# Kernel optimization log

Measured on AMD Instinct MI355X. Metric: run time of the kernel, lower is better.

## Reference

```python
import jax, jax.numpy as jnp
import numpy as np

B, N, C = 8, 8192, 512
H, DH = 8, C // 8
SCALE = 0.02


def setup_inputs() -> dict:
    key = jax.random.key(0)
    k0, k1, k2, k3, k4 = jax.random.split(key, 5)
    return {
        "x": jax.random.normal(k0, (B, N, C), dtype=jnp.float32),
        "w1": SCALE * jax.random.normal(k1, (2, H, DH, DH), dtype=jnp.float32),
        "b1": SCALE * jax.random.normal(k2, (2, H, DH), dtype=jnp.float32),
        "w2": SCALE * jax.random.normal(k3, (2, H, DH, DH), dtype=jnp.float32),
        "b2": SCALE * jax.random.normal(k4, (2, H, DH), dtype=jnp.float32),
    }


def reference(x, w1, b1, w2, b2):
    dtype = x.dtype
    x = x.astype(jnp.float32)
    b, n, c = x.shape
    xf = jnp.fft.rfft(x, axis=1, norm="ortho")            # [B, N//2+1, C] complex
    xf = xf.reshape(b, n // 2 + 1, H, DH)                  # [B, F, H, DH]
    xr, xi = jnp.real(xf), jnp.imag(xf)
    # per-head complex linear 1 + GELU (complex mult split into real/imag)
    o1r = jax.nn.gelu(
        jnp.einsum("bfhi,hio->bfho", xr, w1[0])
        - jnp.einsum("bfhi,hio->bfho", xi, w1[1]) + b1[0], approximate=False)
    o1i = jax.nn.gelu(
        jnp.einsum("bfhi,hio->bfho", xi, w1[0])
        + jnp.einsum("bfhi,hio->bfho", xr, w1[1]) + b1[1], approximate=False)
    # per-head complex linear 2
    o2r = (jnp.einsum("bfhi,hio->bfho", o1r, w2[0])
           - jnp.einsum("bfhi,hio->bfho", o1i, w2[1]) + b2[0])
    o2i = (jnp.einsum("bfhi,hio->bfho", o1i, w2[0])
           + jnp.einsum("bfhi,hio->bfho", o1r, w2[1]) + b2[1])
    yf = (o2r + 1j * o2i).reshape(b, n // 2 + 1, c)
    y = jnp.fft.irfft(yf, n=n, axis=1, norm="ortho")
    return y.astype(dtype)
```

## Files before the change

kernel.cpp:

```cpp
#include <hip/hip_runtime.h>
#include <math.h>

#define BB    8
#define NLEN  8192
#define CC    512
#define HH    8
#define DH    64
#define MH    4096
#define FREQ  4097
#define FP    4104
#define NSEQ  (BB*CC)

#define REGION_BYTES ((size_t)NSEQ * FP * 4ull)

static __device__ __align__(256) unsigned char g_scratch[2ull * (size_t)NSEQ * FP * 4ull];
__device__ unsigned short g_wprep[8 * 4 * 64 * 64];

typedef __attribute__((ext_vector_type(8))) short bf16x8;
typedef __attribute__((ext_vector_type(4))) float f32x4;

__device__ __forceinline__ f32x4 MFMA(bf16x8 a, bf16x8 b, f32x4 c){
  return __builtin_amdgcn_mfma_f32_16x16x32_bf16(a, b, c, 0, 0, 0);
}

__device__ __forceinline__ unsigned short f2bf(float f){
  unsigned u = __float_as_uint(f);
  return (unsigned short)((u + 0x7fffu + ((u >> 16) & 1u)) >> 16);
}
__device__ __forceinline__ unsigned pack2(float a, float b){
  return (unsigned)f2bf(a) | ((unsigned)f2bf(b) << 16);
}
__device__ __forceinline__ float bflo(unsigned u){ return __uint_as_float(u << 16); }
__device__ __forceinline__ float bfhi(unsigned u){ return __uint_as_float(u & 0xffff0000u); }

__device__ __forceinline__ float gelu_fast(float v){
  float x  = v * 0.70710678118654752440f;
  float ax = fabsf(x);
  float t  = __builtin_amdgcn_rcpf(fmaf(0.3275911f, ax, 1.0f));
  float p  = fmaf(fmaf(fmaf(fmaf(1.061405429f, t, -1.453152027f), t,
                            1.421413741f), t, -0.284496736f), t, 0.254829592f);
  float e  = __expf(-x * x);
  float erf_ax = fmaf(-p * t, e, 1.0f);
  float erfx = copysignf(erf_ax, x);
  return 0.5f * v * (1.0f + erfx);
}

__device__ __forceinline__ float2 cadd(float2 a, float2 b){ return make_float2(a.x+b.x, a.y+b.y); }
__device__ __forceinline__ float2 csub(float2 a, float2 b){ return make_float2(a.x-b.x, a.y-b.y); }
__device__ __forceinline__ float2 cmul(float2 a, float2 b){
  return make_float2(fmaf(a.x, b.x, -(a.y*b.y)), fmaf(a.x, b.y, a.y*b.x));
}

__global__ __launch_bounds__(256) void transpose_in_k(const float* __restrict__ in,
                                                      unsigned* __restrict__ out){
  __shared__ float tile[64][33];
  int b  = blockIdx.z;
  int c0 = blockIdx.x * 32;
  int n0 = blockIdx.y * 64;
  int t  = threadIdx.x;
  int tx = t & 31, ty = t >> 5;
  const float* src = in + ((size_t)b * NLEN + n0) * CC + c0;
  #pragma unroll
  for (int k = 0; k < 8; ++k)
    tile[ty + 8*k][tx] = src[(size_t)(ty + 8*k) * CC + tx];
  __syncthreads();
  int lt = t & 15;
  int nl = 4 * lt;
  #pragma unroll
  for (int kk = 0; kk < 2; ++kk){
    int cl = (t >> 4) + 16*kk;
    uint2 u;
    u.x = pack2(tile[nl    ][cl], tile[nl + 1][cl]);
    u.y = pack2(tile[nl + 2][cl], tile[nl + 3][cl]);
    *(uint2*)(out + ((size_t)(b * CC + c0 + cl) * NLEN + n0) / 2 + 2*lt) = u;
  }
}

__global__ __launch_bounds__(256) void transpose_out_k(const unsigned* __restrict__ in,
                                                       float* __restrict__ out){
  __shared__ float tile[64][33];
  int b  = blockIdx.z;
  int c0 = blockIdx.x * 32;
  int n0 = blockIdx.y * 64;
  int t  = threadIdx.x;
  int lt = t & 15;
  int nl = 4 * lt;
  #pragma unroll
  for (int kk = 0; kk < 2; ++kk){
    int cl = (t >> 4) + 16*kk;
    uint2 u = *(const uint2*)(in + ((size_t)(b * CC + c0 + cl) * NLEN + n0) / 2 + 2*lt);
    tile[nl    ][cl] = bflo(u.x);
    tile[nl + 1][cl] = bfhi(u.x);
    tile[nl + 2][cl] = bflo(u.y);
    tile[nl + 3][cl] = bfhi(u.y);
  }
  __syncthreads();
  int tx = t & 31, ty = t >> 5;
  float* dst = out + ((size_t)b * NLEN + n0) * CC + c0;
  #pragma unroll
  for (int k = 0; k < 8; ++k)
    dst[(size_t)(ty + 8*k) * CC + tx] = tile[ty + 8*k][tx];
}

#define SL(e) ((e) + ((e) >> 4))
#define PERM16(p) ((((p) & 3) << 2) | ((p) >> 2))

template<int SIGN>
__device__ __forceinline__ void dft4ip(float2& v0, float2& v1, float2& v2, float2& v3){
  float2 s02 = cadd(v0, v2), d02 = csub(v0, v2);
  float2 s13 = cadd(v1, v3), d13 = csub(v1, v3);
  float2 id = make_float2(-(float)SIGN * d13.y, (float)SIGN * d13.x);
  v0 = cadd(s02, s13);
  v1 = cadd(d02, id);
  v2 = csub(s02, s13);
  v3 = csub(d02, id);
}

template<int SIGN>
__device__ __forceinline__ float2 w16c(int m){
  const float c1 = 0.9238795325112867f, s1 = 0.3826834323650898f, r = 0.7071067811865476f;
  float cs = 1.f, sn = 0.f;
  if (m == 1){ cs = c1;  sn = s1; }
  else if (m == 2){ cs = r;   sn = r; }
  else if (m == 3){ cs = s1;  sn = c1; }
  else if (m == 4){ cs = 0.f; sn = 1.f; }
  else if (m == 6){ cs = -r;  sn = r; }
  else if (m == 9){ cs = -c1; sn = -s1; }
  return make_float2(cs, (float)SIGN * sn);
}

template<int SIGN>
__device__ __forceinline__ void dft16ip(float2 v[16]){
  #pragma unroll
  for (int q0 = 0; q0 < 4; ++q0) dft4ip<SIGN>(v[q0], v[q0+4], v[q0+8], v[q0+12]);
  #pragma unroll
  for (int p0 = 0; p0 < 4; ++p0)
    #pragma unroll
    for (int q0 = 0; q0 < 4; ++q0){
      const int m = p0 * q0;
      if (m) v[q0 + 4*p0] = cmul(v[q0 + 4*p0], w16c<SIGN>(m));
    }
  #pragma unroll
  for (int p0 = 0; p0 < 4; ++p0) dft4ip<SIGN>(v[4*p0], v[4*p0+1], v[4*p0+2], v[4*p0+3]);
}

template<int SIGN>
__device__ __forceinline__ void twiddle16(float2 v[16], int jm, float invRNs){
  float ang = (float)SIGN * 6.2831853071795864769f * (float)jm * invRNs;
  float sn, cs; __sincosf(ang, &sn, &cs);
  float2 w1 = make_float2(cs, sn), w = w1;
  #pragma unroll
  for (int q = 1; q < 16; ++q){ v[q] = cmul(v[q], w); w = cmul(w, w1); }
}

template<int SIGN, int NS>
__device__ __forceinline__ void fft_mid_pass(float2* lds2, float2 v[16], int t){
  #pragma unroll
  for (int q = 0; q < 16; ++q) v[q] = lds2[SL(t + 256*q)];
  int jm = t & (NS - 1);
  twiddle16<SIGN>(v, jm, 1.0f / (16.0f * (float)NS));
  dft16ip<SIGN>(v);
  __syncthreads();
  int base = ((t - jm) << 4) + jm;
  #pragma unroll
  for (int p = 0; p < 16; ++p) lds2[SL(base + p*NS)] = v[PERM16(p)];
  __syncthreads();
}

#define ORTHO_S 0.011048543456039806f

__global__ __launch_bounds__(256) void fft_fwd_k(const unsigned* __restrict__ xt,
                                                 unsigned* __restrict__ spec){
  __shared__ float2 lds2[4352];
  int t = threadIdx.x;
  size_t row = blockIdx.x;
  const unsigned* src = xt + row * (NLEN/2);
  float2 v[16];
  #pragma unroll
  for (int q = 0; q < 16; ++q){
    unsigned u = src[t + 256*q];
    v[q] = make_float2(bflo(u), bfhi(u));
  }
  dft16ip<-1>(v);
  #pragma unroll
  for (int p = 0; p < 16; ++p) lds2[SL(16*t + p)] = v[PERM16(p)];
  __syncthreads();
  fft_mid_pass<-1, 16 >(lds2, v, t);
  fft_mid_pass<-1, 256>(lds2, v, t);
  unsigned* dst = spec + row * (size_t)FP;
  #pragma unroll
  for (int q = 0; q < 16; ++q){
    int k = t + 256*q;
    float2 zk = lds2[SL(k)];
    float2 zc = lds2[SL((MH - k) & (MH - 1))];
    float ex = 0.5f*(zk.x + zc.x);
    float ey = 0.5f*(zk.y - zc.y);
    float ux = zk.x - zc.x;
    float uy = zk.y + zc.y;
    float ox =  0.5f*uy;
    float oy = -0.5f*ux;
    float ang = -6.2831853071795864769f * (float)k / (float)NLEN;
    float sn, cs; __sincosf(ang, &sn, &cs);
    float xr = ex + cs*ox - sn*oy;
    float xi = ey + cs*oy + sn*ox;
    dst[k] = pack2(ORTHO_S*xr, ORTHO_S*xi);
  }
  if (t == 0){
    float2 z0 = lds2[SL(0)];
    dst[MH] = pack2(ORTHO_S*(z0.x - z0.y), 0.0f);
  }
}

__global__ __launch_bounds__(256) void fft_inv_k(const unsigned* __restrict__ spec,
                                                 unsigned* __restrict__ yt){
  __shared__ float2 lds2[4352];
  int t = threadIdx.x;
  size_t row = blockIdx.x;
  const unsigned* src = spec + row * (size_t)FP;
  float2 v[16];
  #pragma unroll
  for (int q = 0; q < 16; ++q){
    int k = t + 256*q;
    unsigned uk = src[k];
    unsigned uc = src[MH - k];
    float2 xk = make_float2(bflo(uk), bfhi(uk));
    float2 xc = make_float2(bflo(uc), bfhi(uc));
    if (k == 0){ xk.y = 0.0f; xc.y = 0.0f; }
    float ex = xk.x + xc.x;
    float ey = xk.y - xc.y;
    float dx = xk.x - xc.x;
    float dy = xk.y + xc.y;
    float ang = 6.2831853071795864769f * (float)k / (float)NLEN;
    float sn, cs; __sincosf(ang, &sn, &cs);
    float ox = cs*dx - sn*dy;
    float oy = cs*dy + sn*dx;
    v[q] = make_float2(ex - oy, ey + ox);
  }
  dft16ip<1>(v);
  #pragma unroll
  for (int p = 0; p < 16; ++p) lds2[SL(16*t + p)] = v[PERM16(p)];
  __syncthreads();
  fft_mid_pass<1, 16 >(lds2, v, t);
  fft_mid_pass<1, 256>(lds2, v, t);
  unsigned* dst = yt + row * (NLEN/2);
  #pragma unroll
  for (int q = 0; q < 16; ++q){
    int m = t + 256*q;
    float2 w = lds2[SL(m)];
    dst[m] = pack2(ORTHO_S*w.x, ORTHO_S*w.y);
  }
}

__global__ __launch_bounds__(256) void wprep_k(const float* __restrict__ w1,
                                               const float* __restrict__ w2){
  int t = threadIdx.x;
  int h = blockIdx.x;
  #pragma unroll 4
  for (int u = 0; u < 64; ++u){
    int idx = t + 256*u;
    int p = idx >> 12;
    int o = (idx >> 6) & 63;
    int jj = idx & 63;
    int swo = (o ^ (o >> 3)) & 7;
    int s = (((jj >> 3) ^ swo) << 3) | (jj & 7);
    int i;
    if (p < 2){
      i = s;
    } else {
      int ks = s >> 5, g = (s >> 3) & 3, j = s & 7;
      i = (2*ks + (j >> 2))*16 + 4*g + (j & 3);
    }
    const float* src = (p < 2) ? w1 : w2;
    float v = src[(size_t)(p & 1) * 32768 + (size_t)h * 4096 + i * 64 + o];
    g_wprep[(size_t)h * 16384 + idx] = f2bf(v);
  }
}

__global__ __launch_bounds__(256) void afno_mid_mfma_k(const unsigned* __restrict__ spec_in,
                                                       unsigned* __restrict__ spec_out,
                                                       const float* __restrict__ b1,
                                                       const float* __restrict__ b2){
  __shared__ unsigned short lds[24576];
  const int t  = threadIdx.x;
  const int bx = blockIdx.x, h = blockIdx.y, b = blockIdx.z;
  const int F0 = bx * 64;
  const size_t rowbase = ((size_t)b * HH + h) * DH;
  const int l = t & 63, wv = t >> 6;
  const int lf = l & 15, lg = l >> 4;

  {
    const uint4* gw  = (const uint4*)(g_wprep + (size_t)h * 16384);
    uint4*       sw4 = (uint4*)(lds + 8192);
    #pragma unroll
    for (int u = 0; u < 8; ++u) sw4[t + 256*u] = gw[t + 256*u];
  }
  {
    unsigned u0[8], u1[8];
    #pragma unroll
    for (int it = 0; it < 8; ++it){
      int ci = wv + 4*it;
      int fc = ci & 3, pc = ci >> 2;
      int f  = fc*16 + lf;
      int i0 = pc*8 + lg*2;
      int fglob = F0 + f;
      u0[it] = 0; u1[it] = 0;
      if (fglob < FREQ){
        u0[it] = spec_in[(rowbase + i0    ) * (size_t)FP + fglob];
        u1[it] = spec_in[(rowbase + i0 + 1) * (size_t)FP + fglob];
      }
    }
    #pragma unroll
    for (int it = 0; it < 8; ++it){
      int ci = wv + 4*it;
      int fc = ci & 3, pc = ci >> 2;
      int f  = fc*16 + lf;
      int i0 = pc*8 + lg*2;
      unsigned wr = __builtin_amdgcn_perm(u1[it], u0[it], 0x05040100u);
      unsigned wi = __builtin_amdgcn_perm(u1[it], u0[it], 0x07060302u);
      int swf = (f ^ (f >> 3)) & 7;
      int j0  = ((((i0 >> 3) ^ swf) << 3) | (i0 & 7));
      *(unsigned*)(lds        + f*64 + j0) = wr;
      *(unsigned*)(lds + 4096 + f*64 + j0) = wi;
    }
  }
  __syncthreads();

  const int wf0 = wv * 16;
  const unsigned short* XR  = lds;
  const unsigned short* XI  = lds + 4096;
  const unsigned short* W1R = lds + 8192;
  const unsigned short* W1I = lds + 12288;
  const unsigned short* W2R = lds + 16384;
  const unsigned short* W2I = lds + 20480;

  const f32x4 zz = {0.f, 0.f, 0.f, 0.f};
  f32x4 a1R[4], a1I[4];
  #pragma unroll
  for (int mt = 0; mt < 4; ++mt){ a1R[mt] = zz; a1I[mt] = zz; }

  #pragma unroll
  for (int ks = 0; ks < 2; ++ks){
    int b0 = ks*4 + lg;
    int f  = wf0 + lf;
    int swf = (f ^ (f >> 3)) & 7;
    int offx = f*64 + ((b0 ^ swf) << 3);
    bf16x8 bxr = *(const bf16x8*)(XR + offx);
    bf16x8 bxi = *(const bf16x8*)(XI + offx);
    #pragma unroll
    for (int mt = 0; mt < 4; ++mt){
      int o = mt*16 + lf;
      int swo = (o ^ (o >> 3)) & 7;
      int off = o*64 + ((b0 ^ swo) << 3);
      bf16x8 awr  = *(const bf16x8*)(W1R + off);
      bf16x8 awi  = *(const bf16x8*)(W1I + off);
      bf16x8 awin = awi ^ (short)0x8000;
      a1R[mt] = MFMA(awr,  bxr, a1R[mt]);
      a1R[mt] = MFMA(awin, bxi, a1R[mt]);
      a1I[mt] = MFMA(awi,  bxr, a1I[mt]);
      a1I[mt] = MFMA(awr,  bxi, a1I[mt]);
    }
  }

  bf16x8 aFr[2], aFi[2], aFin[2];
  #pragma unroll
  for (int ks = 0; ks < 2; ++ks){
    unsigned wr_[4], wi_[4];
    #pragma unroll
    for (int half = 0; half < 2; ++half){
      int mt = 2*ks + half;
      float4 br = *(const float4*)(b1 +       (size_t)h*64 + mt*16 + lg*4);
      float4 bi = *(const float4*)(b1 + 512 + (size_t)h*64 + mt*16 + lg*4);
      float vr0 = gelu_fast(a1R[mt][0] + br.x), vr1 = gelu_fast(a1R[mt][1] + br.y);
      float vr2 = gelu_fast(a1R[mt][2] + br.z), vr3 = gelu_fast(a1R[mt][3] + br.w);
      float vi0 = gelu_fast(a1I[mt][0] + bi.x), vi1 = gelu_fast(a1I[mt][1] + bi.y);
      float vi2 = gelu_fast(a1I[mt][2] + bi.z), vi3 = gelu_fast(a1I[mt][3] + bi.w);
      wr_[half*2    ] = pack2(vr0, vr1);
      wr_[half*2 + 1] = pack2(vr2, vr3);
      wi_[half*2    ] = pack2(vi0, vi1);
      wi_[half*2 + 1] = pack2(vi2, vi3);
    }
    unsigned* pr = (unsigned*)&aFr[ks];
    unsigned* pi = (unsigned*)&aFi[ks];
    #pragma unroll
    for (int w = 0; w < 4; ++w){ pr[w] = wr_[w]; pi[w] = wi_[w]; }
    aFin[ks] = aFi[ks] ^ (short)0x8000;
  }

  f32x4 a2R[4], a2I[4];
  #pragma unroll
  for (int nt = 0; nt < 4; ++nt){ a2R[nt] = zz; a2I[nt] = zz; }

  #pragma unroll
  for (int ks = 0; ks < 2; ++ks){
    int b0 = ks*4 + lg;
    #pragma unroll
    for (int nt = 0; nt < 4; ++nt){
      int o2 = nt*16 + lf;
      int swo = (o2 ^ (o2 >> 3)) & 7;
      int off = o2*64 + ((b0 ^ swo) << 3);
      bf16x8 bwr = *(const bf16x8*)(W2R + off);
      bf16x8 bwi = *(const bf16x8*)(W2I + off);
      a2R[nt] = MFMA(aFr[ks],  bwr, a2R[nt]);
      a2R[nt] = MFMA(aFin[ks], bwi, a2R[nt]);
      a2I[nt] = MFMA(aFi[ks],  bwr, a2I[nt]);
      a2I[nt] = MFMA(aFr[ks],  bwi, a2I[nt]);
    }
  }

  int f0 = F0 + wf0 + lg*4;
  if (f0 <= MH){
    #pragma unroll
    for (int nt = 0; nt < 4; ++nt){
      int o2 = nt*16 + lf;
      float b2r = b2[(size_t)h*64 + o2];
      float b2i = b2[512 + (size_t)h*64 + o2];
      uint4 st;
      st.x = pack2(a2R[nt][0] + b2r, a2I[nt][0] + b2i);
      st.y = pack2(a2R[nt][1] + b2r, a2I[nt][1] + b2i);
      st.z = pack2(a2R[nt][2] + b2r, a2I[nt][2] + b2i);
      st.w = pack2(a2R[nt][3] + b2r, a2I[nt][3] + b2i);
      *(uint4*)(spec_out + (rowbase + o2) * (size_t)FP + f0) = st;
    }
  }
}

extern "C" void kernel_launch(void* const* d_in, const int* in_sizes, int n_in,
                              void* d_out, int out_size, void* d_ws, size_t ws_size,
                              hipStream_t stream) {
  const float* x  = (const float*)d_in[0];
  const float* w1 = (const float*)d_in[1];
  const float* b1 = (const float*)d_in[2];
  const float* w2 = (const float*)d_in[3];
  const float* b2 = (const float*)d_in[4];
  float* out = (float*)d_out;

  unsigned char* base = (unsigned char*)d_ws;
  if (ws_size < 2 * REGION_BYTES){
    void* p = nullptr;
    hipGetSymbolAddress(&p, HIP_SYMBOL(g_scratch));
    base = (unsigned char*)p;
  }
  unsigned* specA = (unsigned*)base;
  unsigned char* regB = base + REGION_BYTES;
  unsigned* xt    = (unsigned*)regB;
  unsigned* specB = (unsigned*)regB;
  unsigned* ytp   = (unsigned*)base;

  wprep_k<<<8, 256, 0, stream>>>(w1, w2);
  transpose_in_k<<<dim3(CC/32, NLEN/64, BB), 256, 0, stream>>>(x, xt);
  fft_fwd_k<<<NSEQ, 256, 0, stream>>>(xt, specA);
  afno_mid_mfma_k<<<dim3(65, HH, BB), 256, 0, stream>>>(specA, specB, b1, b2);
  fft_inv_k<<<NSEQ, 256, 0, stream>>>(specB, ytp);
  transpose_out_k<<<dim3(CC/32, NLEN/64, BB), 256, 0, stream>>>(ytp, out);
}
```

Baseline: 213.7 us.

## Cut sincos calls in FFT kernels and read MLP weights directly from global

The FFT twiddle chain changes from a serial complex-multiply recurrence to a binary-split product tree, which shortens the dependency chain. The per-element sincos in the real-FFT pre/post-processing is replaced by one sincos per thread, rotated by a constant table of 32nd roots of unity. The AFNO MLP kernel stops staging the per-head weights in LDS and loads them straight from global/L2, shrinking LDS from 48KB to 16KB. All three kernels also get launch_bounds min-blocks of 4. Together these aim to cut transcendental work and raise occupancy, at the cost of more global traffic for the weights and possible register pressure or spills.

```diff
diff --git a/kernel.cpp b/kernel.cpp
--- a/kernel.cpp
+++ b/kernel.cpp
@@ -32,6 +32,15 @@
 }
 __device__ __forceinline__ float bflo(unsigned u){ return __uint_as_float(u << 16); }
 __device__ __forceinline__ float bfhi(unsigned u){ return __uint_as_float(u & 0xffff0000u); }
+
+__device__ const float C32C[16] = {
+  1.f, 0.98078528f, 0.92387953f, 0.83146961f, 0.70710678f, 0.55557023f,
+  0.38268343f, 0.19509032f, 0.f, -0.19509032f, -0.38268343f, -0.55557023f,
+  -0.70710678f, -0.83146961f, -0.92387953f, -0.98078528f};
+__device__ const float C32S[16] = {
+  0.f, 0.19509032f, 0.38268343f, 0.55557023f, 0.70710678f, 0.83146961f,
+  0.92387953f, 0.98078528f, 1.f, 0.98078528f, 0.92387953f, 0.83146961f,
+  0.70710678f, 0.55557023f, 0.38268343f, 0.19509032f};
 
 __device__ __forceinline__ float gelu_fast(float v){
   float x  = v * 0.70710678118654752440f;
@@ -148,9 +157,12 @@
 __device__ __forceinline__ void twiddle16(float2 v[16], int jm, float invRNs){
   float ang = (float)SIGN * 6.2831853071795864769f * (float)jm * invRNs;
   float sn, cs; __sincosf(ang, &sn, &cs);
-  float2 w1 = make_float2(cs, sn), w = w1;
-  #pragma unroll
-  for (int q = 1; q < 16; ++q){ v[q] = cmul(v[q], w); w = cmul(w, w1); }
+  float2 tw[16];
+  tw[1] = make_float2(cs, sn);
+  #pragma unroll
+  for (int q = 2; q < 16; ++q) tw[q] = cmul(tw[q >> 1], tw[q - (q >> 1)]);
+  #pragma unroll
+  for (int q = 1; q < 16; ++q) v[q] = cmul(v[q], tw[q]);
 }
 
 template<int SIGN, int NS>
@@ -169,8 +181,8 @@
 
 #define ORTHO_S 0.011048543456039806f
 
-__global__ __launch_bounds__(256) void fft_fwd_k(const unsigned* __restrict__ xt,
-                                                 unsigned* __restrict__ spec){
+__global__ __launch_bounds__(256, 4) void fft_fwd_k(const unsigned* __restrict__ xt,
+                                                    unsigned* __restrict__ spec){
   __shared__ float2 lds2[4352];
   int t = threadIdx.x;
   size_t row = blockIdx.x;
@@ -188,6 +200,8 @@
   fft_mid_pass<-1, 16 >(lds2, v, t);
   fft_mid_pass<-1, 256>(lds2, v, t);
   unsigned* dst = spec + row * (size_t)FP;
+  float snb, csb;
+  __sincosf(-6.2831853071795864769f * (float)t / (float)NLEN, &snb, &csb);
   #pragma unroll
   for (int q = 0; q < 16; ++q){
     int k = t + 256*q;
@@ -199,8 +213,8 @@
     float uy = zk.y + zc.y;
     float ox =  0.5f*uy;
     float oy = -0.5f*ux;
-    float ang = -6.2831853071795864769f * (float)k / (float)NLEN;
-    float sn, cs; __sincosf(ang, &sn, &cs);
+    float cs = fmaf(csb, C32C[q],  snb*C32S[q]);
+    float sn = fmaf(snb, C32C[q], -csb*C32S[q]);
     float xr = ex + cs*ox - sn*oy;
     float xi = ey + cs*oy + sn*ox;
     dst[k] = pack2(ORTHO_S*xr, ORTHO_S*xi);
@@ -211,13 +225,15 @@
   }
 }
 
-__global__ __launch_bounds__(256) void fft_inv_k(const unsigned* __restrict__ spec,
-                                                 unsigned* __restrict__ yt){
+__global__ __launch_bounds__(256, 4) void fft_inv_k(const unsigned* __restrict__ spec,
+                                                    unsigned* __restrict__ yt){
   __shared__ float2 lds2[4352];
   int t = threadIdx.x;
   size_t row = blockIdx.x;
   const unsigned* src = spec + row * (size_t)FP;
   float2 v[16];
+  float snb, csb;
+  __sincosf(6.2831853071795864769f * (float)t / (float)NLEN, &snb, &csb);
   #pragma unroll
   for (int q = 0; q < 16; ++q){
     int k = t + 256*q;
@@ -230,8 +246,8 @@
     float ey = xk.y - xc.y;
     float dx = xk.x - xc.x;
     float dy = xk.y + xc.y;
-    float ang = 6.2831853071795864769f * (float)k / (float)NLEN;
-    float sn, cs; __sincosf(ang, &sn, &cs);
+    float cs = fmaf(csb, C32C[q], -snb*C32S[q]);
+    float sn = fmaf(snb, C32C[q],  csb*C32S[q]);
     float ox = cs*dx - sn*dy;
     float oy = cs*dy + sn*dx;
     v[q] = make_float2(ex - oy, ey + ox);
@@ -276,24 +292,19 @@
   }
 }
 
-__global__ __launch_bounds__(256) void afno_mid_mfma_k(const unsigned* __restrict__ spec_in,
-                                                       unsigned* __restrict__ spec_out,
-                                                       const float* __restrict__ b1,
-                                                       const float* __restrict__ b2){
-  __shared__ unsigned short lds[24576];
+__global__ __launch_bounds__(256, 4) void afno_mid_mfma_k(const unsigned* __restrict__ spec_in,
+                                                          unsigned* __restrict__ spec_out,
+                                                          const float* __restrict__ b1,
+                                                          const float* __restrict__ b2){
+  __shared__ unsigned short lds[8192];
   const int t  = threadIdx.x;
   const int bx = blockIdx.x, h = blockIdx.y, b = blockIdx.z;
   const int F0 = bx * 64;
   const size_t rowbase = ((size_t)b * HH + h) * DH;
   const int l = t & 63, wv = t >> 6;
   const int lf = l & 15, lg = l >> 4;
-
-  {
-    const uint4* gw  = (const uint4*)(g_wprep + (size_t)h * 16384);
-    uint4*       sw4 = (uint4*)(lds + 8192);
-    #pragma unroll
-    for (int u = 0; u < 8; ++u) sw4[t + 256*u] = gw[t + 256*u];
-  }
+  const unsigned short* __restrict__ W = g_wprep + (size_t)h * 16384;
+
   {
     unsigned u0[8], u1[8];
     #pragma unroll
@@ -328,10 +339,6 @@
   const int wf0 = wv * 16;
   const unsigned short* XR  = lds;
   const unsigned short* XI  = lds + 4096;
-  const unsigned short* W1R = lds + 8192;
-  const unsigned short* W1I = lds + 12288;
-  const unsigned short* W2R = lds + 16384;
-  const unsigned short* W2I = lds + 20480;
 
   const f32x4 zz = {0.f, 0.f, 0.f, 0.f};
   f32x4 a1R[4], a1I[4];
@@ -351,8 +358,8 @@
       int o = mt*16 + lf;
       int swo = (o ^ (o >> 3)) & 7;
       int off = o*64 + ((b0 ^ swo) << 3);
-      bf16x8 awr  = *(const bf16x8*)(W1R + off);
-      bf16x8 awi  = *(const bf16x8*)(W1I + off);
+      bf16x8 awr  = *(const bf16x8*)(W + off);
+      bf16x8 awi  = *(const bf16x8*)(W + 4096 + off);
       bf16x8 awin = awi ^ (short)0x8000;
       a1R[mt] = MFMA(awr,  bxr, a1R[mt]);
       a1R[mt] = MFMA(awin, bxi, a1R[mt]);
@@ -398,8 +405,8 @@
       int o2 = nt*16 + lf;
       int swo = (o2 ^ (o2 >> 3)) & 7;
       int off = o2*64 + ((b0 ^ swo) << 3);
-      bf16x8 bwr = *(const bf16x8*)(W2R + off);
-      bf16x8 bwi = *(const bf16x8*)(W2I + off);
+      bf16x8 bwr = *(const bf16x8*)(W + 8192  + off);
+      bf16x8 bwi = *(const bf16x8*)(W + 12288 + off);
       a2R[nt] = MFMA(aFr[ks],  bwr, a2R[nt]);
       a2R[nt] = MFMA(aFin[ks], bwi, a2R[nt]);
       a2I[nt] = MFMA(aFi[ks],  bwr, a2I[nt]);
```

Result: slower. 219.7 us (+2.8%).
